# Kernel tuning notes

Hardware: AMD Instinct MI355X
Metric: run time of the kernel (lower is better)

Reference implementation:

```python
import jax, jax.numpy as jnp
import numpy as np

N_NODES = 50000
N_EDGES = 800000
D_IN, D_HID, D_OUT = 128, 256, 256


def _sage_conv(x, src, dst, w_l, b_l, w_r, n_nodes):
    # PyG SAGEConv (mean aggr): out = lin_l(mean_{j in N(i)} x_j) + lin_r(x_i)
    # lin_l has bias, lin_r has no bias.
    msg_sum = jax.ops.segment_sum(x[src], dst, num_segments=n_nodes)  # [N, d]
    deg = jax.ops.segment_sum(jnp.ones_like(dst, dtype=x.dtype), dst, num_segments=n_nodes)
    agg = msg_sum / jnp.maximum(deg, 1.0)[:, None]
    return agg @ w_l.T + b_l + x @ w_r.T


def setup_inputs() -> dict:
    key = jax.random.key(0)
    ks = jax.random.split(key, 8)
    x = jax.random.normal(ks[0], (N_NODES, D_IN), dtype=jnp.float32)
    edge_index = jax.random.randint(ks[1], (2, N_EDGES), 0, N_NODES, dtype=jnp.int64)
    s1 = 1.0 / np.sqrt(D_IN)
    s2 = 1.0 / np.sqrt(D_HID)
    w_l1 = jax.random.uniform(ks[2], (D_HID, D_IN), jnp.float32, -s1, s1)
    b_l1 = jax.random.uniform(ks[3], (D_HID,), jnp.float32, -s1, s1)
    w_r1 = jax.random.uniform(ks[4], (D_HID, D_IN), jnp.float32, -s1, s1)
    w_l2 = jax.random.uniform(ks[5], (D_OUT, D_HID), jnp.float32, -s2, s2)
    b_l2 = jax.random.uniform(ks[6], (D_OUT,), jnp.float32, -s2, s2)
    w_r2 = jax.random.uniform(ks[7], (D_OUT, D_HID), jnp.float32, -s2, s2)
    return {"x": x, "edge_index": edge_index,
            "w_l1": w_l1, "b_l1": b_l1, "w_r1": w_r1,
            "w_l2": w_l2, "b_l2": b_l2, "w_r2": w_r2}


def reference(x, edge_index, w_l1, b_l1, w_r1, w_l2, b_l2, w_r2):
    src, dst = edge_index[0], edge_index[1]
    h = jax.nn.relu(_sage_conv(x, src, dst, w_l1, b_l1, w_r1, N_NODES))
    out = jax.nn.relu(_sage_conv(h, src, dst, w_l2, b_l2, w_r2, N_NODES))
    return out
```

## Files before the change

### kernel.cpp

```cpp
#include <hip/hip_runtime.h>
#include <hip/hip_fp16.h>
#include <stdint.h>

#define N_NODES 50000
#define N_EDGES 800000
#define BCAP 64
#define NPART 782
#define NSUB 4
#define SCAP 384

typedef _Float16 f16x8 __attribute__((ext_vector_type(8)));
typedef __attribute__((ext_vector_type(4))) float f32x4;

__device__ __forceinline__ unsigned short f2h(float f) {
    return __builtin_bit_cast(unsigned short, (_Float16)f);
}

__device__ __forceinline__ unsigned char f2fp8o(float v) {
    v = fminf(v, 440.f) + 0.015625f;
    unsigned int u = __builtin_bit_cast(unsigned int, v);
    u += 0x7FFFFu + ((u >> 20) & 1u);
    return (unsigned char)((u >> 20) - 960u);
}

__device__ __forceinline__ void load_lds16(const void* g, void* l) {
    __builtin_amdgcn_global_load_lds(
        (const __attribute__((address_space(1))) void*)(uintptr_t)g,
        (__attribute__((address_space(3))) void*)(unsigned int)(uintptr_t)l,
        16, 0, 0);
}

__global__ __launch_bounds__(256) void part_append_k(
    const int* __restrict__ src, const int* __restrict__ dst,
    int* __restrict__ pcnt, unsigned int* __restrict__ pbuf, int nedges)
{
    int e = blockIdx.x * 256 + threadIdx.x;
    if (e >= nedges) return;
    int s = src[e], d = dst[e];
    int cidx = (d >> 6) * NSUB + (e & (NSUB - 1));
    int pos = atomicAdd(&pcnt[cidx * 16], 1);
    if (pos < SCAP)
        pbuf[(size_t)cidx * SCAP + pos] = ((unsigned)(d & 63) << 16) | (unsigned)s;
}

__global__ __launch_bounds__(256) void part_bucket_k(
    const int* __restrict__ pcnt, const unsigned int* __restrict__ pbuf,
    int* __restrict__ bucket, int* __restrict__ degtot, float* __restrict__ invdeg)
{
    __shared__ int lcnt[64];
    int part = blockIdx.x, tid = threadIdx.x;
    if (tid < 64) lcnt[tid] = 0;
    __syncthreads();
#pragma unroll
    for (int sub = 0; sub < NSUB; sub++) {
        int cidx = part * NSUB + sub;
        int n = pcnt[cidx * 16];
        if (n > SCAP) n = SCAP;
        const unsigned int* pb = pbuf + (size_t)cidx * SCAP;
        for (int i = tid; i < n; i += 256) {
            unsigned int en = pb[i];
            int dlow = (int)(en >> 16), s = (int)(en & 0xFFFFu);
            int p = atomicAdd(&lcnt[dlow], 1);
            if (p < BCAP) bucket[(size_t)(part * 64 + dlow) * BCAP + p] = s;
        }
    }
    __syncthreads();
    if (tid < 64) {
        int node = part * 64 + tid;
        if (node < N_NODES) {
            int c = lcnt[tid];
            degtot[node] = (c > BCAP) ? BCAP : c;
            invdeg[node] = 1.0f / (float)(c > 1 ? c : 1);
        }
    }
}

__global__ __launch_bounds__(256) void cvt_x_k(
    const float* __restrict__ x, unsigned short* __restrict__ dst)
{
    int tid = blockIdx.x * 256 + threadIdx.x;
    if (tid >= N_NODES * 32) return;
    int row = tid >> 5, c = (tid & 31) * 4;
    float4 v = *(const float4*)(x + (size_t)row * 128 + c);
    ushort4 o;
    o.x = f2h(v.x); o.y = f2h(v.y); o.z = f2h(v.z); o.w = f2h(v.w);
    *(ushort4*)(dst + (size_t)row * 256 + 128 + c) = o;
}

__global__ __launch_bounds__(256) void cvt_w_k(
    const float* __restrict__ wl, const float* __restrict__ wr,
    unsigned short* __restrict__ dst, int Keach)
{
    int tid = blockIdx.x * 256 + threadIdx.x;
    if (tid >= 256 * 2 * Keach) return;
    int n = tid / (2 * Keach), k = tid - n * 2 * Keach;
    float v = (k < Keach) ? wl[(size_t)n * Keach + k]
                          : wr[(size_t)n * Keach + (k - Keach)];
    dst[tid] = f2h(v);
}

__device__ __forceinline__ void acch4(__half2* a, uint4 u) {
    a[0] = __hadd2(a[0], __builtin_bit_cast(__half2, u.x));
    a[1] = __hadd2(a[1], __builtin_bit_cast(__half2, u.y));
    a[2] = __hadd2(a[2], __builtin_bit_cast(__half2, u.z));
    a[3] = __hadd2(a[3], __builtin_bit_cast(__half2, u.w));
}

__global__ __launch_bounds__(256) void agg1_k(
    const unsigned short* __restrict__ feat,
    const int* __restrict__ bucket, const int* __restrict__ degtot,
    const float* __restrict__ invdeg,
    unsigned short* __restrict__ outmsg)
{
    int wv = threadIdx.x >> 6, lane = threadIdx.x & 63;
    int node = blockIdx.x * 4 + wv;
    if (node >= N_NODES) return;
    int deg = degtot[node];
    int idx0 = bucket[(size_t)node * BCAP + lane];
    const int sub = lane >> 4;
    const int col = lane & 15;

    __half2 acc[4] = {};
    auto rowp = [&](int s) { return (const uint4*)(feat + (size_t)s * 256 + col * 8); };

    int j = 0;
    for (; j + 16 <= deg; j += 16) {
        int s0 = __shfl(idx0, j + sub),     s1 = __shfl(idx0, j + 4 + sub);
        int s2 = __shfl(idx0, j + 8 + sub), s3 = __shfl(idx0, j + 12 + sub);
        uint4 u0 = *rowp(s0), u1 = *rowp(s1), u2 = *rowp(s2), u3 = *rowp(s3);
        acch4(acc, u0); acch4(acc, u1); acch4(acc, u2); acch4(acc, u3);
    }
    for (; j + 8 <= deg; j += 8) {
        int s0 = __shfl(idx0, j + sub), s1 = __shfl(idx0, j + 4 + sub);
        uint4 u0 = *rowp(s0), u1 = *rowp(s1);
        acch4(acc, u0); acch4(acc, u1);
    }
    for (; j + 4 <= deg; j += 4) {
        uint4 u0 = *rowp(__shfl(idx0, j + sub));
        acch4(acc, u0);
    }
    if (j < deg) {
        int e = j + sub;
        int ec = (e < deg) ? e : (deg - 1);
        uint4 u0 = *rowp(__shfl(idx0, ec));
        if (e < deg) acch4(acc, u0);
    }
#pragma unroll
    for (int stride = 32; stride >= 16; stride >>= 1)
#pragma unroll
        for (int v = 0; v < 4; v++) {
            int t = __shfl_xor(__builtin_bit_cast(int, acc[v]), stride);
            acc[v] = __hadd2(acc[v], __builtin_bit_cast(__half2, t));
        }

    if (lane < 16) {
        float s = invdeg[node];
        unsigned int o[4];
#pragma unroll
        for (int v = 0; v < 4; v++) {
            float2 f = __half22float2(acc[v]);
            o[v] = (unsigned int)f2h(f.x * s) | ((unsigned int)f2h(f.y * s) << 16);
        }
        *(uint4*)(outmsg + (size_t)node * 256 + lane * 8) = make_uint4(o[0], o[1], o[2], o[3]);
    }
}

__device__ __forceinline__ void accf8pk(__half2* a, unsigned int w) {
    unsigned int ev = ((w & 0x00FF00FFu) << 7) + 0x20002000u;
    unsigned int od = ((w >> 1) & 0x7F807F80u) + 0x20002000u;
    a[0] = __hadd2(a[0], __builtin_bit_cast(__half2, ev));
    a[1] = __hadd2(a[1], __builtin_bit_cast(__half2, od));
}
__device__ __forceinline__ void accf8x16(__half2* a, uint4 u) {
    accf8pk(a + 0, u.x); accf8pk(a + 2, u.y); accf8pk(a + 4, u.z); accf8pk(a + 6, u.w);
}

__global__ __launch_bounds__(256) void agg2_k(
    const unsigned char* __restrict__ hf8,
    const int* __restrict__ bucket, const int* __restrict__ degtot,
    const float* __restrict__ invdeg,
    unsigned short* __restrict__ outmsg)
{
    int wv = threadIdx.x >> 6, lane = threadIdx.x & 63;
    int node = blockIdx.x * 4 + wv;
    if (node >= N_NODES) return;
    int deg = degtot[node];
    int idx0 = bucket[(size_t)node * BCAP + lane];
    const int sub = lane >> 4;
    const int col = lane & 15;

    __half2 acc[8] = {};
    auto rowp = [&](int s) { return (const uint4*)(hf8 + (size_t)s * 256 + col * 16); };

    int j = 0;
    for (; j + 16 <= deg; j += 16) {
        int s0 = __shfl(idx0, j + sub),     s1 = __shfl(idx0, j + 4 + sub);
        int s2 = __shfl(idx0, j + 8 + sub), s3 = __shfl(idx0, j + 12 + sub);
        uint4 u0 = *rowp(s0), u1 = *rowp(s1), u2 = *rowp(s2), u3 = *rowp(s3);
        accf8x16(acc, u0); accf8x16(acc, u1); accf8x16(acc, u2); accf8x16(acc, u3);
    }
    for (; j + 8 <= deg; j += 8) {
        int s0 = __shfl(idx0, j + sub), s1 = __shfl(idx0, j + 4 + sub);
        uint4 u0 = *rowp(s0), u1 = *rowp(s1);
        accf8x16(acc, u0); accf8x16(acc, u1);
    }
    for (; j + 4 <= deg; j += 4) {
        uint4 u0 = *rowp(__shfl(idx0, j + sub));
        accf8x16(acc, u0);
    }
    if (j < deg) {
        int e = j + sub;
        int ec = (e < deg) ? e : (deg - 1);
        uint4 u0 = *rowp(__shfl(idx0, ec));
        if (e < deg) accf8x16(acc, u0);
    }
#pragma unroll
    for (int stride = 32; stride >= 16; stride >>= 1)
#pragma unroll
        for (int v = 0; v < 8; v++) {
            int t = __shfl_xor(__builtin_bit_cast(int, acc[v]), stride);
            acc[v] = __hadd2(acc[v], __builtin_bit_cast(__half2, t));
        }

    if (lane < 16) {
        float s = invdeg[node];
        float bias = (deg > 0) ? 0.015625f : 0.0f;
        unsigned int o[8];
#pragma unroll
        for (int q = 0; q < 4; q++) {
            float2 ev = __half22float2(acc[2 * q]);
            float2 od = __half22float2(acc[2 * q + 1]);
            float d0 = ev.x * s - bias, d1 = od.x * s - bias;
            float d2 = ev.y * s - bias, d3 = od.y * s - bias;
            o[2 * q]     = (unsigned int)f2h(d0) | ((unsigned int)f2h(d1) << 16);
            o[2 * q + 1] = (unsigned int)f2h(d2) | ((unsigned int)f2h(d3) << 16);
        }
        unsigned short* wp = outmsg + (size_t)node * 512 + lane * 16;
        *(uint4*)(wp)     = make_uint4(o[0], o[1], o[2], o[3]);
        *(uint4*)(wp + 8) = make_uint4(o[4], o[5], o[6], o[7]);
    }
}

template <bool F16OUT, bool WRITE_FP8>
__global__ __launch_bounds__(256) void gemm_k(
    const unsigned short* __restrict__ A, const unsigned short* __restrict__ W,
    const float* __restrict__ bias, void* __restrict__ outp, int outStride,
    unsigned char* __restrict__ hf8, int M, int K)
{
    __shared__ __align__(16) char smem[2 * 16384];
    const int t = threadIdx.x;
    const int w = t >> 6, lane = t & 63;
    const int quad = lane >> 4, l15 = lane & 15;
    const int row0 = blockIdx.x * 128;
    const int col0 = blockIdx.y * 128;
    const int niter = K >> 5;

    auto stage = [&](int buf, int ks) {
#pragma unroll
        for (int j = 0; j < 4; j++) {
            int call = w * 4 + j;
            int ci = call * 64 + lane;
            const unsigned short* g;
            if (call < 8) {
                int rg = row0 + (ci >> 2);
                if (rg > M - 1) rg = M - 1;
                g = A + (size_t)rg * K + ks + (ci & 3) * 8;
            } else {
                int c2 = ci - 512;
                g = W + (size_t)(col0 + (c2 >> 2)) * K + ks + (c2 & 3) * 8;
            }
            load_lds16(g, smem + buf * 16384 + ci * 16);
        }
    };

    f32x4 acc[2][8] = {};

    stage(0, 0);
    __syncthreads();

    for (int i = 0; i < niter; i++) {
        if (i + 1 < niter) stage((i + 1) & 1, (i + 1) << 5);

        const char* base = smem + (i & 1) * 16384;
        const char* Ab = base + (w * 32 + l15) * 64 + quad * 16;
        const char* Wb = base + 8192 + l15 * 64 + quad * 16;
        f16x8 af0 = *(const f16x8*)(Ab);
        f16x8 af1 = *(const f16x8*)(Ab + 1024);
#pragma unroll
        for (int tt = 0; tt < 8; tt++) {
            f16x8 bfr = *(const f16x8*)(Wb + tt * 1024);
            acc[0][tt] = __builtin_amdgcn_mfma_f32_16x16x32_f16(af0, bfr, acc[0][tt], 0, 0, 0);
            acc[1][tt] = __builtin_amdgcn_mfma_f32_16x16x32_f16(af1, bfr, acc[1][tt], 0, 0, 0);
        }
        __syncthreads();
    }

#pragma unroll
    for (int g = 0; g < 2; g++) {
#pragma unroll
        for (int tt = 0; tt < 8; tt++) {
            int col = col0 + tt * 16 + l15;
            float bv = bias[col];
#pragma unroll
            for (int i = 0; i < 4; i++) {
                int row = row0 + w * 32 + g * 16 + quad * 4 + i;
                if (row < M) {
                    float v = fmaxf(acc[g][tt][i] + bv, 0.f);
                    size_t off = (size_t)row * outStride + col;
                    if constexpr (F16OUT) ((unsigned short*)outp)[off] = f2h(v);
                    else                  ((float*)outp)[off] = v;
                    if constexpr (WRITE_FP8) hf8[(size_t)row * 256 + col] = f2fp8o(v);
                }
            }
        }
    }
}

extern "C" void kernel_launch(void* const* d_in, const int* in_sizes, int n_in,
                              void* d_out, int out_size, void* d_ws, size_t ws_size,
                              hipStream_t stream)
{
    const float* x   = (const float*)d_in[0];
    const int*   ei  = (const int*)d_in[1];
    const float* wl1 = (const float*)d_in[2];
    const float* bl1 = (const float*)d_in[3];
    const float* wr1 = (const float*)d_in[4];
    const float* wl2 = (const float*)d_in[5];
    const float* bl2 = (const float*)d_in[6];
    const float* wr2 = (const float*)d_in[7];
    float* out = (float*)d_out;
    const int* src = ei;
    const int* dst = ei + N_EDGES;

    char* ws = (char*)d_ws;
    size_t off = 0;
    auto alloc = [&](size_t bytes) -> void* {
        void* p = ws + off;
        off = (off + bytes + 255) & ~(size_t)255;
        return p;
    };
    int*            pcnt   = (int*)           alloc((size_t)NPART * NSUB * 16 * 4);
    unsigned int*   pbuf   = (unsigned int*)  alloc((size_t)NPART * NSUB * SCAP * 4);
    int*            bucket = (int*)           alloc((size_t)NPART * 64 * BCAP * 4);
    int*            degtot = (int*)           alloc((size_t)N_NODES * 4);
    float*          invdeg = (float*)         alloc((size_t)N_NODES * 4);
    unsigned short* Acat1  = (unsigned short*)alloc((size_t)N_NODES * 256 * 2);
    unsigned short* Acat2  = (unsigned short*)alloc((size_t)N_NODES * 512 * 2);
    unsigned char*  hf8    = (unsigned char*) alloc((size_t)N_NODES * 256);
    unsigned short* Wcat1  = (unsigned short*)alloc((size_t)256 * 256 * 2);
    unsigned short* Wcat2  = (unsigned short*)alloc((size_t)256 * 512 * 2);

    hipMemsetAsync(pcnt, 0, (size_t)NPART * NSUB * 16 * 4, stream);
    part_append_k<<<(N_EDGES + 255) / 256, 256, 0, stream>>>(src, dst, pcnt, pbuf, N_EDGES);
    part_bucket_k<<<NPART, 256, 0, stream>>>(pcnt, pbuf, bucket, degtot, invdeg);

    cvt_x_k<<<(N_NODES * 32 + 255) / 256, 256, 0, stream>>>(x, Acat1);
    cvt_w_k<<<(256 * 256 + 255) / 256, 256, 0, stream>>>(wl1, wr1, Wcat1, 128);
    cvt_w_k<<<(256 * 512 + 255) / 256, 256, 0, stream>>>(wl2, wr2, Wcat2, 256);

    agg1_k<<<(N_NODES + 3) / 4, 256, 0, stream>>>(
        Acat1 + 128, bucket, degtot, invdeg, Acat1);
    gemm_k<true, true><<<dim3((N_NODES + 127) / 128, 2), 256, 0, stream>>>(
        Acat1, Wcat1, bl1, (void*)(Acat2 + 256), 512, hf8, N_NODES, 256);

    agg2_k<<<(N_NODES + 3) / 4, 256, 0, stream>>>(
        hf8, bucket, degtot, invdeg, Acat2);
    gemm_k<false, false><<<dim3((N_NODES + 127) / 128, 2), 256, 0, stream>>>(
        Acat2, Wcat2, bl2, (void*)out, 256, nullptr, N_NODES, 512);
}
```

Baseline: 279.4 us.

## Triple-buffer GEMM staging, fragment-ordered LDS, and widen edge partitioning

The GEMM moves from double to triple LDS buffering with two stages in flight, explicit vmcnt waits and a single barrier per iteration. It also stores tiles in fragment order so each lane reads one contiguous 16-byte chunk, avoiding LDS bank conflicts. Edge partitioning now uses 16 sub-buckets of 128 slots to spread atomic contention, each thread handles four edges with vectorized loads, and the bucket kernel assigns one wavefront per sub-bucket. These changes raise LDS use and rely on hand-counted vmcnt values; the smaller per-sub-bucket capacity may overflow and drop edges on skewed graphs.

```diff
diff --git a/kernel.cpp b/kernel.cpp
--- a/kernel.cpp
+++ b/kernel.cpp
@@ -6,8 +6,8 @@
 #define N_EDGES 800000
 #define BCAP 64
 #define NPART 782
-#define NSUB 4
-#define SCAP 384
+#define NSUB 16
+#define SCAP 128
 
 typedef _Float16 f16x8 __attribute__((ext_vector_type(8)));
 typedef __attribute__((ext_vector_type(4))) float f32x4;
@@ -34,13 +34,26 @@
     const int* __restrict__ src, const int* __restrict__ dst,
     int* __restrict__ pcnt, unsigned int* __restrict__ pbuf, int nedges)
 {
-    int e = blockIdx.x * 256 + threadIdx.x;
-    if (e >= nedges) return;
-    int s = src[e], d = dst[e];
-    int cidx = (d >> 6) * NSUB + (e & (NSUB - 1));
-    int pos = atomicAdd(&pcnt[cidx * 16], 1);
-    if (pos < SCAP)
-        pbuf[(size_t)cidx * SCAP + pos] = ((unsigned)(d & 63) << 16) | (unsigned)s;
+    int t = blockIdx.x * 256 + threadIdx.x;
+    int e0 = t * 4;
+    if (e0 >= nedges) return;
+    int4 s4 = *(const int4*)(src + e0);
+    int4 d4 = *(const int4*)(dst + e0);
+
+    int c0 = (d4.x >> 6) * NSUB + ((e0 + 0) & (NSUB - 1));
+    int c1 = (d4.y >> 6) * NSUB + ((e0 + 1) & (NSUB - 1));
+    int c2 = (d4.z >> 6) * NSUB + ((e0 + 2) & (NSUB - 1));
+    int c3 = (d4.w >> 6) * NSUB + ((e0 + 3) & (NSUB - 1));
+
+    int p0 = atomicAdd(&pcnt[c0 * 16], 1);
+    int p1 = atomicAdd(&pcnt[c1 * 16], 1);
+    int p2 = atomicAdd(&pcnt[c2 * 16], 1);
+    int p3 = atomicAdd(&pcnt[c3 * 16], 1);
+
+    if (p0 < SCAP) pbuf[(size_t)c0 * SCAP + p0] = ((unsigned)(d4.x & 63) << 16) | (unsigned)s4.x;
+    if (p1 < SCAP) pbuf[(size_t)c1 * SCAP + p1] = ((unsigned)(d4.y & 63) << 16) | (unsigned)s4.y;
+    if (p2 < SCAP) pbuf[(size_t)c2 * SCAP + p2] = ((unsigned)(d4.z & 63) << 16) | (unsigned)s4.z;
+    if (p3 < SCAP) pbuf[(size_t)c3 * SCAP + p3] = ((unsigned)(d4.w & 63) << 16) | (unsigned)s4.w;
 }
 
 __global__ __launch_bounds__(256) void part_bucket_k(
@@ -49,15 +62,16 @@
 {
     __shared__ int lcnt[64];
     int part = blockIdx.x, tid = threadIdx.x;
+    int wv = tid >> 6, lane = tid & 63;
     if (tid < 64) lcnt[tid] = 0;
     __syncthreads();
 #pragma unroll
-    for (int sub = 0; sub < NSUB; sub++) {
+    for (int sub = wv; sub < NSUB; sub += 4) {
         int cidx = part * NSUB + sub;
         int n = pcnt[cidx * 16];
         if (n > SCAP) n = SCAP;
         const unsigned int* pb = pbuf + (size_t)cidx * SCAP;
-        for (int i = tid; i < n; i += 256) {
+        for (int i = lane; i < n; i += 64) {
             unsigned int en = pb[i];
             int dlow = (int)(en >> 16), s = (int)(en & 0xFFFFu);
             int p = atomicAdd(&lcnt[dlow], 1);
@@ -247,7 +261,7 @@
     const float* __restrict__ bias, void* __restrict__ outp, int outStride,
     unsigned char* __restrict__ hf8, int M, int K)
 {
-    __shared__ __align__(16) char smem[2 * 16384];
+    __shared__ __align__(16) char smem[3 * 16384];
     const int t = threadIdx.x;
     const int w = t >> 6, lane = t & 63;
     const int quad = lane >> 4, l15 = lane & 15;
@@ -255,44 +269,52 @@
     const int col0 = blockIdx.y * 128;
     const int niter = K >> 5;
 
-    auto stage = [&](int buf, int ks) {
+    auto stage = [&](char* dstbuf, int ks) {
 #pragma unroll
         for (int j = 0; j < 4; j++) {
-            int call = w * 4 + j;
-            int ci = call * 64 + lane;
+            int c = j * 256 + t;
+            int cl = c & 63, frag = c >> 6;
+            int fl = cl & 15, fq = cl >> 4;
             const unsigned short* g;
-            if (call < 8) {
-                int rg = row0 + (ci >> 2);
-                if (rg > M - 1) rg = M - 1;
-                g = A + (size_t)rg * K + ks + (ci & 3) * 8;
+            if (frag < 8) {
+                int rr = row0 + (frag >> 1) * 32 + (frag & 1) * 16 + fl;
+                if (rr > M - 1) rr = M - 1;
+                g = A + (size_t)rr * K + ks + fq * 8;
             } else {
-                int c2 = ci - 512;
-                g = W + (size_t)(col0 + (c2 >> 2)) * K + ks + (c2 & 3) * 8;
+                int tt = frag - 8;
+                g = W + (size_t)(col0 + tt * 16 + fl) * K + ks + fq * 8;
             }
-            load_lds16(g, smem + buf * 16384 + ci * 16);
+            load_lds16(g, dstbuf + c * 16);
         }
     };
 
     f32x4 acc[2][8] = {};
 
-    stage(0, 0);
-    __syncthreads();
+    char* curp = smem;
+    char* stgp = smem + 2 * 16384;
+    stage(smem, 0);
+    stage(smem + 16384, 32);
 
     for (int i = 0; i < niter; i++) {
-        if (i + 1 < niter) stage((i + 1) & 1, (i + 1) << 5);
-
-        const char* base = smem + (i & 1) * 16384;
-        const char* Ab = base + (w * 32 + l15) * 64 + quad * 16;
-        const char* Wb = base + 8192 + l15 * 64 + quad * 16;
-        f16x8 af0 = *(const f16x8*)(Ab);
-        f16x8 af1 = *(const f16x8*)(Ab + 1024);
+        if (i < niter - 1) asm volatile("s_waitcnt vmcnt(4)" ::: "memory");
+        else               asm volatile("s_waitcnt vmcnt(0)" ::: "memory");
+        __builtin_amdgcn_s_barrier();
+        __builtin_amdgcn_sched_barrier(0);
+
+        if (i + 2 < niter) stage(stgp, (i + 2) << 5);
+
+        const char* Ab = curp + (w * 2) * 1024 + lane * 16;
+        f16x8 a0 = *(const f16x8*)(Ab);
+        f16x8 a1 = *(const f16x8*)(Ab + 1024);
+        const char* Wb = curp + 8192 + lane * 16;
 #pragma unroll
         for (int tt = 0; tt < 8; tt++) {
             f16x8 bfr = *(const f16x8*)(Wb + tt * 1024);
-            acc[0][tt] = __builtin_amdgcn_mfma_f32_16x16x32_f16(af0, bfr, acc[0][tt], 0, 0, 0);
-            acc[1][tt] = __builtin_amdgcn_mfma_f32_16x16x32_f16(af1, bfr, acc[1][tt], 0, 0, 0);
-        }
-        __syncthreads();
+            acc[0][tt] = __builtin_amdgcn_mfma_f32_16x16x32_f16(a0, bfr, acc[0][tt], 0, 0, 0);
+            acc[1][tt] = __builtin_amdgcn_mfma_f32_16x16x32_f16(a1, bfr, acc[1][tt], 0, 0, 0);
+        }
+        curp += 16384; if (curp == smem + 49152) curp = smem;
+        stgp += 16384; if (stgp == smem + 49152) stgp = smem;
     }
 
 #pragma unroll
@@ -351,7 +373,7 @@
     unsigned short* Wcat2  = (unsigned short*)alloc((size_t)256 * 512 * 2);
 
     hipMemsetAsync(pcnt, 0, (size_t)NPART * NSUB * 16 * 4, stream);
-    part_append_k<<<(N_EDGES + 255) / 256, 256, 0, stream>>>(src, dst, pcnt, pbuf, N_EDGES);
+    part_append_k<<<(N_EDGES / 4 + 255) / 256, 256, 0, stream>>>(src, dst, pcnt, pbuf, N_EDGES);
     part_bucket_k<<<NPART, 256, 0, stream>>>(pcnt, pbuf, bucket, degtot, invdeg);
 
     cvt_x_k<<<(N_NODES * 32 + 255) / 256, 256, 0, stream>>>(x, Acat1);
```

Result: slower. 290.1 us (+3.9%).
